# Kernel tuning notes

Hardware: AMD Instinct MI355X
Metric: run time of the kernel (lower is better)

The kernel has to match this reference:

```python
import jax, jax.numpy as jnp
import numpy as np

EMBED_SIZE = 768
HEAD_SIZE = 64
B, T = 4, 2048


def setup_inputs() -> dict:
    key = jax.random.key(0)
    kx, kk, kq, kv = jax.random.split(key, 4)
    x = jax.random.normal(kx, (B, T, EMBED_SIZE), dtype=jnp.float32)
    # torch Linear(E, H, bias=False): weight [H, E]; stored here as [E, H] for x @ W
    s = 1.0 / np.sqrt(EMBED_SIZE)
    Wk = jax.random.uniform(kk, (EMBED_SIZE, HEAD_SIZE), jnp.float32, -s, s)
    Wq = jax.random.uniform(kq, (EMBED_SIZE, HEAD_SIZE), jnp.float32, -s, s)
    Wv = jax.random.uniform(kv, (EMBED_SIZE, HEAD_SIZE), jnp.float32, -s, s)
    return {"x": x, "Wk": Wk, "Wq": Wq, "Wv": Wv}


def reference(x, Wk, Wq, Wv):
    Bx, Tx, E = x.shape
    k = x @ Wk  # [B, T, H]
    q = x @ Wq
    v = x @ Wv
    w = jnp.einsum("bth,bsh->bts", q, k)  # [B, T, T]
    causal = jnp.tril(jnp.ones((Tx, Tx), dtype=bool))
    # Faithful to source: mask to -inf FIRST, then scale by sqrt(embed_size)
    w = jnp.where(causal, w, -jnp.inf)
    w = w / jnp.sqrt(jnp.asarray(E, dtype=x.dtype))
    w = jax.nn.softmax(w, axis=-1)
    # dropout: eval mode / identity for the correctness baseline
    return jnp.einsum("bts,bsh->bth", w, v)
```

## Files before the change

kernel.cpp:

```cpp
#include <hip/hip_runtime.h>
#include <hip/hip_bf16.h>


typedef __attribute__((ext_vector_type(8))) short short8;
typedef __attribute__((ext_vector_type(4))) float f32x4;

#define SPLIT_KB 4
#define MAX_SP 8

__device__ __forceinline__ unsigned short f2bf(float f) {
    union { float f; unsigned u; } v; v.f = f;
    unsigned r = v.u + 0x7fffu + ((v.u >> 16) & 1u);
    return (unsigned short)(r >> 16);
}

__global__ __launch_bounds__(512) void proj_kernel(const float* __restrict__ x,
                                                   const float* __restrict__ Wk,
                                                   const float* __restrict__ Wq,
                                                   const float* __restrict__ Wv,
                                                   unsigned short* __restrict__ qws,
                                                   unsigned short* __restrict__ kws,
                                                   unsigned short* __restrict__ vT) {
    __shared__ unsigned short xs[32 * 72];
    __shared__ unsigned short wsm[192 * 72];
    const float CSCALE = 1.4426950408889634f / 27.712812921102035f;
    int tid = threadIdx.x;
    int lane = tid & 63, wave = tid >> 6;
    int quad = lane >> 4, l16 = lane & 15;
    int wm = wave & 1, wn2 = wave >> 1;
    int row0 = blockIdx.x * 32;

    int xrow = tid >> 4, xcb = (tid & 15) * 4;
    int wn = tid & 63, wk0 = (tid >> 6) * 8;

    f32x4 acc[3];
    for (int nt = 0; nt < 3; ++nt) acc[nt] = (f32x4)(0.f);

    for (int kc = 0; kc < 12; ++kc) {
        __syncthreads();
        {
            const float* src = x + (size_t)(row0 + xrow) * 768 + kc * 64 + xcb;
            float4 f0 = *(const float4*)(src);
            unsigned short p0 = f2bf(f0.x), p1 = f2bf(f0.y),
                           p2 = f2bf(f0.z), p3 = f2bf(f0.w);
            unsigned short* d = &xs[xrow * 72 + xcb];
            d[0] = p0; d[1] = p1; d[2] = p2; d[3] = p3;
        }
        for (int my = 0; my < 3; ++my) {
            const float* W = (my == 0) ? Wq : (my == 1) ? Wk : Wv;
            float wv[8];
            for (int i = 0; i < 8; ++i)
                wv[i] = W[(size_t)(kc * 64 + wk0 + i) * 64 + wn];
            if (my == 0)
                for (int i = 0; i < 8; ++i) wv[i] *= CSCALE;
            short8 p;
            for (int i = 0; i < 8; ++i) p[i] = (short)f2bf(wv[i]);
            *(short8*)&wsm[(my * 64 + wn) * 72 + wk0] = p;
        }
        __syncthreads();
        for (int kh = 0; kh < 2; ++kh) {
            int kk = kh * 32 + quad * 8;
            short8 a = *(const short8*)&xs[(wm * 16 + l16) * 72 + kk];
            for (int nt = 0; nt < 3; ++nt) {
                short8 bfr = *(const short8*)&wsm[(wn2 * 48 + nt * 16 + l16) * 72 + kk];
                acc[nt] = __builtin_amdgcn_mfma_f32_16x16x32_bf16(a, bfr, acc[nt], 0, 0, 0);
            }
        }
    }
    __syncthreads();
    for (int nt = 0; nt < 3; ++nt) {
        int n = wn2 * 48 + nt * 16 + l16;
        int mat = n >> 6, col = n & 63;
        for (int j = 0; j < 4; ++j) {
            int rloc = wm * 16 + quad * 4 + j;
            unsigned short bv = f2bf(acc[nt][j]);
            if (mat == 0)      qws[(size_t)(row0 + rloc) * 64 + col] = bv;
            else if (mat == 1) kws[(size_t)(row0 + rloc) * 64 + col] = bv;
            else               wsm[col * 40 + rloc] = bv;
        }
    }
    __syncthreads();
    if (tid < 256) {
        int bidx = row0 >> 11, t0 = row0 & 2047;
        int c = tid >> 2, rb = (tid & 3) * 8;
        *(short8*)&vT[((size_t)(bidx * 64 + c)) * 2048 + t0 + rb] =
            *(const short8*)&wsm[c * 40 + rb];
    }
}

__global__ __launch_bounds__(64) void attn_split(const unsigned short* __restrict__ qws,
                                                 const unsigned short* __restrict__ kws,
                                                 const unsigned short* __restrict__ vT,
                                                 float* __restrict__ po,
                                                 float* __restrict__ pm,
                                                 float* __restrict__ pl,
                                                 float* __restrict__ out) {
    int bx = blockIdx.x, b = blockIdx.y, sp = blockIdx.z;
    int kbmax = (bx >> 2) + 1;
    int nsp = (kbmax + SPLIT_KB - 1) / SPLIT_KB;
    if (sp >= nsp) return;
    int kb_lo = sp * SPLIT_KB;
    int kb_hi = min(kb_lo + SPLIT_KB, kbmax);

    __shared__ unsigned short ps[16 * 72];
    int lane = threadIdx.x & 63;
    int quad = lane >> 4, l16 = lane & 15;
    int q0 = bx * 16;

    const unsigned short* qp = qws + ((size_t)b * 2048 + q0 + l16) * 64 + quad * 8;
    short8 aq0 = *(const short8*)(qp);
    short8 aq1 = *(const short8*)(qp + 32);

    f32x4 o_acc[4];
    for (int nt = 0; nt < 4; ++nt) o_acc[nt] = (f32x4)(0.f);
    float m_run[4], l_run[4];
    int row_g[4];
    for (int j = 0; j < 4; ++j) {
        m_run[j] = -1e30f; l_run[j] = 0.f;
        row_g[j] = q0 + quad * 4 + j;
    }

    for (int kb = kb_lo; kb < kb_hi; ++kb) {
        const unsigned short* kp =
            kws + ((size_t)b * 2048 + kb * 64 + l16) * 64 + quad * 8;
        f32x4 s[4];
        for (int nt = 0; nt < 4; ++nt) s[nt] = (f32x4)(0.f);
        for (int nt = 0; nt < 4; ++nt) {
            short8 bk0 = *(const short8*)(kp + (size_t)nt * 16 * 64);
            short8 bk1 = *(const short8*)(kp + (size_t)nt * 16 * 64 + 32);
            s[nt] = __builtin_amdgcn_mfma_f32_16x16x32_bf16(aq0, bk0, s[nt], 0, 0, 0);
            s[nt] = __builtin_amdgcn_mfma_f32_16x16x32_bf16(aq1, bk1, s[nt], 0, 0, 0);
        }
        if (kb == kbmax - 1) {
            for (int nt = 0; nt < 4; ++nt) {
                int key = kb * 64 + nt * 16 + l16;
                for (int j = 0; j < 4; ++j)
                    if (key > row_g[j]) s[nt][j] = -1e30f;
            }
        }
        float mx[4], al[4], rs[4];
        for (int j = 0; j < 4; ++j)
            mx[j] = fmaxf(fmaxf(s[0][j], s[1][j]), fmaxf(s[2][j], s[3][j]));
        for (int off = 1; off < 16; off <<= 1)
            for (int j = 0; j < 4; ++j)
                mx[j] = fmaxf(mx[j], __shfl_xor(mx[j], off, 16));
        for (int j = 0; j < 4; ++j) {
            float mn = fmaxf(m_run[j], mx[j]);
            al[j] = exp2f(m_run[j] - mn);
            m_run[j] = mn;
            rs[j] = 0.f;
        }
        for (int nt = 0; nt < 4; ++nt)
            for (int j = 0; j < 4; ++j) {
                float p = exp2f(s[nt][j] - m_run[j]);
                rs[j] += p;
                ps[(quad * 4 + j) * 72 + nt * 16 + l16] = f2bf(p);
            }
        for (int off = 1; off < 16; off <<= 1)
            for (int j = 0; j < 4; ++j)
                rs[j] += __shfl_xor(rs[j], off, 16);
        for (int j = 0; j < 4; ++j) l_run[j] = l_run[j] * al[j] + rs[j];
        for (int nt = 0; nt < 4; ++nt)
            for (int j = 0; j < 4; ++j) o_acc[nt][j] *= al[j];
        const unsigned short* vp =
            vT + ((size_t)b * 64 + l16) * 2048 + kb * 64 + quad * 8;
        for (int kh = 0; kh < 2; ++kh) {
            short8 ap = *(const short8*)&ps[l16 * 72 + kh * 32 + quad * 8];
            for (int nt = 0; nt < 4; ++nt) {
                short8 bv = *(const short8*)(vp + (size_t)nt * 16 * 2048 + kh * 32);
                o_acc[nt] = __builtin_amdgcn_mfma_f32_16x16x32_bf16(ap, bv, o_acc[nt], 0, 0, 0);
            }
        }
    }
    if (nsp == 1) {
        for (int nt = 0; nt < 4; ++nt)
            for (int j = 0; j < 4; ++j)
                out[((size_t)b * 2048 + row_g[j]) * 64 + nt * 16 + l16] =
                    o_acc[nt][j] / l_run[j];
        return;
    }
    int sbase = ((b * 128 + bx) * MAX_SP + sp) * 16;
    for (int nt = 0; nt < 4; ++nt)
        for (int j = 0; j < 4; ++j) {
            int r = quad * 4 + j;
            po[(size_t)(sbase + r) * 64 + nt * 16 + l16] = o_acc[nt][j];
        }
    if (l16 == 0) {
        for (int j = 0; j < 4; ++j) {
            int r = quad * 4 + j;
            pm[sbase + r] = m_run[j];
            pl[sbase + r] = l_run[j];
        }
    }
}

__global__ __launch_bounds__(256) void reduce_kernel(const float* __restrict__ po,
                                                     const float* __restrict__ pm,
                                                     const float* __restrict__ pl,
                                                     float* __restrict__ out) {
    int tid = threadIdx.x;
    int lane = tid & 63, wave = tid >> 6;
    int g = blockIdx.x * 4 + wave;
    int b = g >> 11, t = g & 2047;
    int bx = t >> 4, r = t & 15;
    int kbmax = (bx >> 2) + 1;
    int nsp = (kbmax + SPLIT_KB - 1) / SPLIT_KB;
    if (nsp == 1) return;
    int base = ((b * 128 + bx) * MAX_SP) * 16 + r;
    float mstar = -1e30f;
    for (int sp = 0; sp < nsp; ++sp)
        mstar = fmaxf(mstar, pm[base + sp * 16]);
    float acc = 0.f, lsum = 0.f;
    for (int sp = 0; sp < nsp; ++sp) {
        float w = exp2f(pm[base + sp * 16] - mstar);
        acc += w * po[(size_t)(base + sp * 16) * 64 + lane];
        lsum += w * pl[base + sp * 16];
    }
    out[(size_t)g * 64 + lane] = acc / lsum;
}

extern "C" void kernel_launch(void* const* d_in, const int* in_sizes, int n_in,
                              void* d_out, int out_size, void* d_ws, size_t ws_size,
                              hipStream_t stream) {
    const float* x  = (const float*)d_in[0];
    const float* Wk = (const float*)d_in[1];
    const float* Wq = (const float*)d_in[2];
    const float* Wv = (const float*)d_in[3];
    float* out = (float*)d_out;
    char* w = (char*)d_ws;
    unsigned short* qws = (unsigned short*)w;
    unsigned short* kws = (unsigned short*)(w + 1048576);
    unsigned short* vT  = (unsigned short*)(w + 2097152);
    float* po = (float*)(w + 3145728);
    float* pm = (float*)(w + 19922944);
    float* pl = (float*)(w + 20185088);
    proj_kernel<<<256, 512, 0, stream>>>(x, Wk, Wq, Wv, qws, kws, vT);
    attn_split<<<dim3(128, 4, MAX_SP), 64, 0, stream>>>(qws, kws, vT, po, pm, pl, out);
    reduce_kernel<<<2048, 256, 0, stream>>>(po, pm, pl, out);
}
```

Measured before the change: 120.2 us.

## Fuse split-K reduction into attention via atomic counter; halve projection tile

The separate reduce kernel is removed. The last attention split block to finish for each query tile, detected with an atomic counter and thread fences, merges the partial outputs itself. The counters are zeroed inside the projection kernel, which now processes 16 rows per block with 256 threads across 512 blocks. This removes one kernel launch and a pass over the partials, but the merge now runs serially over 16 rows inside a single 64-thread block.

```diff
diff --git a/kernel.cpp b/kernel.cpp
--- a/kernel.cpp
+++ b/kernel.cpp
@@ -14,24 +14,29 @@
     return (unsigned short)(r >> 16);
 }
 
-__global__ __launch_bounds__(512) void proj_kernel(const float* __restrict__ x,
+__global__ __launch_bounds__(256) void proj_kernel(const float* __restrict__ x,
                                                    const float* __restrict__ Wk,
                                                    const float* __restrict__ Wq,
                                                    const float* __restrict__ Wv,
                                                    unsigned short* __restrict__ qws,
                                                    unsigned short* __restrict__ kws,
-                                                   unsigned short* __restrict__ vT) {
-    __shared__ unsigned short xs[32 * 72];
+                                                   unsigned short* __restrict__ vT,
+                                                   unsigned* __restrict__ cnt) {
+    __shared__ unsigned short xs[16 * 72];
     __shared__ unsigned short wsm[192 * 72];
     const float CSCALE = 1.4426950408889634f / 27.712812921102035f;
     int tid = threadIdx.x;
     int lane = tid & 63, wave = tid >> 6;
     int quad = lane >> 4, l16 = lane & 15;
-    int wm = wave & 1, wn2 = wave >> 1;
-    int row0 = blockIdx.x * 32;
+    int row0 = blockIdx.x * 16;
+
+    {
+        int g = blockIdx.x * 256 + tid;
+        if (g < 512) cnt[g] = 0;
+    }
 
     int xrow = tid >> 4, xcb = (tid & 15) * 4;
-    int wn = tid & 63, wk0 = (tid >> 6) * 8;
+    int wn = tid & 63, wk0 = (tid >> 6) * 16;
 
     f32x4 acc[3];
     for (int nt = 0; nt < 3; ++nt) acc[nt] = (f32x4)(0.f);
@@ -41,38 +46,41 @@
         {
             const float* src = x + (size_t)(row0 + xrow) * 768 + kc * 64 + xcb;
             float4 f0 = *(const float4*)(src);
-            unsigned short p0 = f2bf(f0.x), p1 = f2bf(f0.y),
-                           p2 = f2bf(f0.z), p3 = f2bf(f0.w);
             unsigned short* d = &xs[xrow * 72 + xcb];
-            d[0] = p0; d[1] = p1; d[2] = p2; d[3] = p3;
+            d[0] = f2bf(f0.x); d[1] = f2bf(f0.y);
+            d[2] = f2bf(f0.z); d[3] = f2bf(f0.w);
         }
         for (int my = 0; my < 3; ++my) {
             const float* W = (my == 0) ? Wq : (my == 1) ? Wk : Wv;
-            float wv[8];
-            for (int i = 0; i < 8; ++i)
+            float wv[16];
+            for (int i = 0; i < 16; ++i)
                 wv[i] = W[(size_t)(kc * 64 + wk0 + i) * 64 + wn];
             if (my == 0)
-                for (int i = 0; i < 8; ++i) wv[i] *= CSCALE;
-            short8 p;
-            for (int i = 0; i < 8; ++i) p[i] = (short)f2bf(wv[i]);
-            *(short8*)&wsm[(my * 64 + wn) * 72 + wk0] = p;
+                for (int i = 0; i < 16; ++i) wv[i] *= CSCALE;
+            short8 p0, p1;
+            for (int i = 0; i < 8; ++i) {
+                p0[i] = (short)f2bf(wv[i]);
+                p1[i] = (short)f2bf(wv[8 + i]);
+            }
+            *(short8*)&wsm[(my * 64 + wn) * 72 + wk0] = p0;
+            *(short8*)&wsm[(my * 64 + wn) * 72 + wk0 + 8] = p1;
         }
         __syncthreads();
         for (int kh = 0; kh < 2; ++kh) {
             int kk = kh * 32 + quad * 8;
-            short8 a = *(const short8*)&xs[(wm * 16 + l16) * 72 + kk];
+            short8 a = *(const short8*)&xs[l16 * 72 + kk];
             for (int nt = 0; nt < 3; ++nt) {
-                short8 bfr = *(const short8*)&wsm[(wn2 * 48 + nt * 16 + l16) * 72 + kk];
+                short8 bfr = *(const short8*)&wsm[(wave * 48 + nt * 16 + l16) * 72 + kk];
                 acc[nt] = __builtin_amdgcn_mfma_f32_16x16x32_bf16(a, bfr, acc[nt], 0, 0, 0);
             }
         }
     }
     __syncthreads();
     for (int nt = 0; nt < 3; ++nt) {
-        int n = wn2 * 48 + nt * 16 + l16;
+        int n = wave * 48 + nt * 16 + l16;
         int mat = n >> 6, col = n & 63;
         for (int j = 0; j < 4; ++j) {
-            int rloc = wm * 16 + quad * 4 + j;
+            int rloc = quad * 4 + j;
             unsigned short bv = f2bf(acc[nt][j]);
             if (mat == 0)      qws[(size_t)(row0 + rloc) * 64 + col] = bv;
             else if (mat == 1) kws[(size_t)(row0 + rloc) * 64 + col] = bv;
@@ -80,9 +88,9 @@
         }
     }
     __syncthreads();
-    if (tid < 256) {
+    if (tid < 128) {
         int bidx = row0 >> 11, t0 = row0 & 2047;
-        int c = tid >> 2, rb = (tid & 3) * 8;
+        int c = tid >> 1, rb = (tid & 1) * 8;
         *(short8*)&vT[((size_t)(bidx * 64 + c)) * 2048 + t0 + rb] =
             *(const short8*)&wsm[c * 40 + rb];
     }
@@ -94,6 +102,7 @@
                                                  float* __restrict__ po,
                                                  float* __restrict__ pm,
                                                  float* __restrict__ pl,
+                                                 unsigned* __restrict__ cnt,
                                                  float* __restrict__ out) {
     int bx = blockIdx.x, b = blockIdx.y, sp = blockIdx.z;
     int kbmax = (bx >> 2) + 1;
@@ -192,31 +201,26 @@
             pl[sbase + r] = l_run[j];
         }
     }
-}
-
-__global__ __launch_bounds__(256) void reduce_kernel(const float* __restrict__ po,
-                                                     const float* __restrict__ pm,
-                                                     const float* __restrict__ pl,
-                                                     float* __restrict__ out) {
-    int tid = threadIdx.x;
-    int lane = tid & 63, wave = tid >> 6;
-    int g = blockIdx.x * 4 + wave;
-    int b = g >> 11, t = g & 2047;
-    int bx = t >> 4, r = t & 15;
-    int kbmax = (bx >> 2) + 1;
-    int nsp = (kbmax + SPLIT_KB - 1) / SPLIT_KB;
-    if (nsp == 1) return;
-    int base = ((b * 128 + bx) * MAX_SP) * 16 + r;
-    float mstar = -1e30f;
-    for (int sp = 0; sp < nsp; ++sp)
-        mstar = fmaxf(mstar, pm[base + sp * 16]);
-    float acc = 0.f, lsum = 0.f;
-    for (int sp = 0; sp < nsp; ++sp) {
-        float w = exp2f(pm[base + sp * 16] - mstar);
-        acc += w * po[(size_t)(base + sp * 16) * 64 + lane];
-        lsum += w * pl[base + sp * 16];
-    }
-    out[(size_t)g * 64 + lane] = acc / lsum;
+    __threadfence();
+    unsigned old = 0;
+    if (lane == 0) old = atomicAdd(&cnt[b * 128 + bx], 1u);
+    old = __shfl(old, 0);
+    if (old == (unsigned)(nsp - 1)) {
+        __threadfence();
+        int base = ((b * 128 + bx) * MAX_SP) * 16;
+        for (int r = 0; r < 16; ++r) {
+            float mstar = -1e30f;
+            for (int s2 = 0; s2 < nsp; ++s2)
+                mstar = fmaxf(mstar, pm[base + s2 * 16 + r]);
+            float acc2 = 0.f, lsum = 0.f;
+            for (int s2 = 0; s2 < nsp; ++s2) {
+                float wgt = exp2f(pm[base + s2 * 16 + r] - mstar);
+                acc2 += wgt * po[(size_t)(base + s2 * 16 + r) * 64 + lane];
+                lsum += wgt * pl[base + s2 * 16 + r];
+            }
+            out[((size_t)b * 2048 + q0 + r) * 64 + lane] = acc2 / lsum;
+        }
+    }
 }
 
 extern "C" void kernel_launch(void* const* d_in, const int* in_sizes, int n_in,
@@ -234,7 +238,7 @@
     float* po = (float*)(w + 3145728);
     float* pm = (float*)(w + 19922944);
     float* pl = (float*)(w + 20185088);
-    proj_kernel<<<256, 512, 0, stream>>>(x, Wk, Wq, Wv, qws, kws, vT);
-    attn_split<<<dim3(128, 4, MAX_SP), 64, 0, stream>>>(qws, kws, vT, po, pm, pl, out);
-    reduce_kernel<<<2048, 256, 0, stream>>>(po, pm, pl, out);
-}
+    unsigned* cnt = (unsigned*)(w + 20447232);
+    proj_kernel<<<512, 256, 0, stream>>>(x, Wk, Wq, Wv, qws, kws, vT, cnt);
+    attn_split<<<dim3(128, 4, MAX_SP), 64, 0, stream>>>(qws, kws, vT, po, pm, pl, cnt, out);
+}
```

New measurement: 246.0 us. +104.6%, slower.
